# Kernel tuning notes

Measured on AMD Instinct MI355X. Metric: run time of the kernel, lower is better.

The kernel has to match this reference:

```python
import jax, jax.numpy as jnp
import numpy as np

C = 96        # channels
NH = 4        # num_heads
WIN = (2, 2, 2)
B, D, H, W = 2, 48, 48, 48
HID = 4 * C   # FFN hidden dim
EPS = 1e-5


def setup_inputs() -> dict:
    key = jax.random.key(0)
    ks = iter(jax.random.split(key, 64))
    def nrm(shape, scale=0.02):
        return jax.random.normal(next(ks), shape, jnp.float32) * scale
    inp = {
        "fg_feature": jax.random.normal(next(ks), (B, C, D, H, W), jnp.float32),
        "bg_feature": jax.random.normal(next(ks), (B, C, D, H, W), jnp.float32),
    }
    for p in ("fg", "bg"):
        inp[f"{p}_qn_w"] = jnp.ones((C,), jnp.float32)
        inp[f"{p}_qn_b"] = jnp.zeros((C,), jnp.float32)
        inp[f"{p}_kvn_w"] = jnp.ones((C,), jnp.float32)
        inp[f"{p}_kvn_b"] = jnp.zeros((C,), jnp.float32)
        inp[f"{p}_attn_in_w"] = nrm((3 * C, C))
        inp[f"{p}_attn_in_b"] = jnp.zeros((3 * C,), jnp.float32)
        inp[f"{p}_attn_out_w"] = nrm((C, C))
        inp[f"{p}_attn_out_b"] = jnp.zeros((C,), jnp.float32)
        inp[f"{p}_ffn_n_w"] = jnp.ones((C,), jnp.float32)
        inp[f"{p}_ffn_n_b"] = jnp.zeros((C,), jnp.float32)
        inp[f"{p}_ffn_w1"] = nrm((HID, C))
        inp[f"{p}_ffn_b1"] = jnp.zeros((HID,), jnp.float32)
        inp[f"{p}_ffn_w2"] = nrm((C, HID))
        inp[f"{p}_ffn_b2"] = jnp.zeros((C,), jnp.float32)
        inp[f"{p}_conv_w"] = nrm((C, C))  # 1x1x1 Conv3d kernel flattened to [Cout,Cin]
        inp[f"{p}_conv_b"] = jnp.zeros((C,), jnp.float32)
        inp[f"{p}_in_w"] = jnp.ones((C,), jnp.float32)
        inp[f"{p}_in_b"] = jnp.zeros((C,), jnp.float32)
    return inp


def _gelu(x):
    return jax.nn.gelu(x, approximate=False)  # torch nn.GELU default (erf)


def _ln(x, w, b):
    m = x.mean(-1, keepdims=True)
    v = ((x - m) ** 2).mean(-1, keepdims=True)
    return (x - m) * jax.lax.rsqrt(v + EPS) * w + b


def _window_partition(x):
    b, c, d, h, w = x.shape
    wd, wh, ww = WIN
    x = x.reshape(b, c, d // wd, wd, h // wh, wh, w // ww, ww)
    x = x.transpose(0, 2, 4, 6, 3, 5, 7, 1)
    return x.reshape(-1, wd * wh * ww, c)  # [num_windows, 8, C]


def _window_reverse(t, shape):
    b, c, d, h, w = shape
    wd, wh, ww = WIN
    x = t.reshape(b, d // wd, h // wh, w // ww, wd, wh, ww, c)
    x = x.transpose(0, 7, 1, 4, 2, 5, 3, 6)
    return x.reshape(b, c, d, h, w)


def _mha(q, k, v, Wi, bi, Wo, bo):
    # torch MultiheadAttention with packed in_proj, batch_first
    N, Lq, c = q.shape
    dh = c // NH
    qp = (q @ Wi[:c].T + bi[:c]).reshape(N, Lq, NH, dh)
    kp = (k @ Wi[c:2 * c].T + bi[c:2 * c]).reshape(N, -1, NH, dh)
    vp = (v @ Wi[2 * c:].T + bi[2 * c:]).reshape(N, -1, NH, dh)
    att = jnp.einsum('nqhd,nkhd->nhqk', qp, kp) * (1.0 / np.sqrt(dh))
    att = jax.nn.softmax(att, axis=-1)
    o = jnp.einsum('nhqk,nkhd->nqhd', att, vp).reshape(N, Lq, c)
    return o @ Wo.T + bo


def _ffn(x, w1, b1, w2, b2):
    return _gelu(x @ w1.T + b1) @ w2.T + b2


def _proj(x, cw, cb, iw, ib):
    # 1x1x1 Conv3d -> InstanceNorm3d(affine) -> GELU
    y = jnp.einsum('bcdhw,oc->bodhw', x, cw) + cb[None, :, None, None, None]
    m = y.mean((2, 3, 4), keepdims=True)
    v = ((y - m) ** 2).mean((2, 3, 4), keepdims=True)
    y = (y - m) * jax.lax.rsqrt(v + EPS)
    y = y * iw[None, :, None, None, None] + ib[None, :, None, None, None]
    return _gelu(y)


def _forward(fg_feature, bg_feature,
             fg_qn_w, fg_qn_b, fg_kvn_w, fg_kvn_b,
             fg_attn_in_w, fg_attn_in_b, fg_attn_out_w, fg_attn_out_b,
             fg_ffn_n_w, fg_ffn_n_b, fg_ffn_w1, fg_ffn_b1, fg_ffn_w2, fg_ffn_b2,
             fg_conv_w, fg_conv_b, fg_in_w, fg_in_b,
             bg_qn_w, bg_qn_b, bg_kvn_w, bg_kvn_b,
             bg_attn_in_w, bg_attn_in_b, bg_attn_out_w, bg_attn_out_b,
             bg_ffn_n_w, bg_ffn_n_b, bg_ffn_w1, bg_ffn_b1, bg_ffn_w2, bg_ffn_b2,
             bg_conv_w, bg_conv_b, bg_in_w, bg_in_b):
    meta = fg_feature.shape
    fg_t = _window_partition(fg_feature)
    bg_t = _window_partition(bg_feature)
    fg_q = _ln(fg_t, fg_qn_w, fg_qn_b)
    bg_q = _ln(bg_t, bg_qn_w, bg_qn_b)
    fg_c = _ln(fg_t, fg_kvn_w, fg_kvn_b)
    bg_c = _ln(bg_t, bg_kvn_w, bg_kvn_b)
    fg_t = fg_t + _mha(fg_q, bg_c, bg_c, fg_attn_in_w, fg_attn_in_b, fg_attn_out_w, fg_attn_out_b)
    bg_t = bg_t + _mha(bg_q, fg_c, fg_c, bg_attn_in_w, bg_attn_in_b, bg_attn_out_w, bg_attn_out_b)
    fg_t = fg_t + _ffn(_ln(fg_t, fg_ffn_n_w, fg_ffn_n_b), fg_ffn_w1, fg_ffn_b1, fg_ffn_w2, fg_ffn_b2)
    bg_t = bg_t + _ffn(_ln(bg_t, bg_ffn_n_w, bg_ffn_n_b), bg_ffn_w1, bg_ffn_b1, bg_ffn_w2, bg_ffn_b2)
    fg = _window_reverse(fg_t, meta)
    bg = _window_reverse(bg_t, meta)
    fg = _proj(fg, fg_conv_w, fg_conv_b, fg_in_w, fg_in_b)
    bg = _proj(bg, bg_conv_w, bg_conv_b, bg_in_w, bg_in_b)
    return fg, bg


def reference(fg_feature, bg_feature,
              fg_qn_w, fg_qn_b, fg_kvn_w, fg_kvn_b,
              fg_attn_in_w, fg_attn_in_b, fg_attn_out_w, fg_attn_out_b,
              fg_ffn_n_w, fg_ffn_n_b, fg_ffn_w1, fg_ffn_b1, fg_ffn_w2, fg_ffn_b2,
              fg_conv_w, fg_conv_b, fg_in_w, fg_in_b,
              bg_qn_w, bg_qn_b, bg_kvn_w, bg_kvn_b,
              bg_attn_in_w, bg_attn_in_b, bg_attn_out_w, bg_attn_out_b,
              bg_ffn_n_w, bg_ffn_n_b, bg_ffn_w1, bg_ffn_b1, bg_ffn_w2, bg_ffn_b2,
              bg_conv_w, bg_conv_b, bg_in_w, bg_in_b):
    return _forward(fg_feature, bg_feature,
                    fg_qn_w, fg_qn_b, fg_kvn_w, fg_kvn_b,
                    fg_attn_in_w, fg_attn_in_b, fg_attn_out_w, fg_attn_out_b,
                    fg_ffn_n_w, fg_ffn_n_b, fg_ffn_w1, fg_ffn_b1, fg_ffn_w2, fg_ffn_b2,
                    fg_conv_w, fg_conv_b, fg_in_w, fg_in_b,
                    bg_qn_w, bg_qn_b, bg_kvn_w, bg_kvn_b,
                    bg_attn_in_w, bg_attn_in_b, bg_attn_out_w, bg_attn_out_b,
                    bg_ffn_n_w, bg_ffn_n_b, bg_ffn_w1, bg_ffn_b1, bg_ffn_w2, bg_ffn_b2,
                    bg_conv_w, bg_conv_b, bg_in_w, bg_in_b)
```

## Files before the change

### kernel.cpp

```cpp
#include <hip/hip_runtime.h>
#include <hip/hip_bf16.h>


#define G_TOK 221184
#define TOK_PER_B 110592
#define STREAM_ELEMS 21233664

typedef __attribute__((ext_vector_type(8))) short short8;
typedef __attribute__((ext_vector_type(4))) float f32x4;
typedef unsigned short ushort_t;
typedef unsigned int uint_t;

#define MFMA16 __builtin_amdgcn_mfma_f32_16x16x32_bf16

__device__ __forceinline__ float gelu_erf(float x) {
    return 0.5f * x * (1.0f + erff(x * 0.70710678118654752f));
}
__device__ __forceinline__ float gelu_tanh(float x) {
    float u = x * (1.5957691216f + 0.0713548163f * x * x);
    return x / (1.0f + __expf(-u));
}
__device__ __forceinline__ ushort_t bfb(float f) {
    __hip_bfloat16 h = __float2bfloat16(f);
    return *reinterpret_cast<ushort_t*>(&h);
}
__device__ __forceinline__ void unpack8(uint4 v, float* o) {
    o[0] = __uint_as_float(v.x << 16); o[1] = __uint_as_float(v.x & 0xffff0000u);
    o[2] = __uint_as_float(v.y << 16); o[3] = __uint_as_float(v.y & 0xffff0000u);
    o[4] = __uint_as_float(v.z << 16); o[5] = __uint_as_float(v.z & 0xffff0000u);
    o[6] = __uint_as_float(v.w << 16); o[7] = __uint_as_float(v.w & 0xffff0000u);
}
__device__ __forceinline__ uint4 pack8(const float* f) {
    uint4 v;
    v.x = (uint_t)bfb(f[0]) | ((uint_t)bfb(f[1]) << 16);
    v.y = (uint_t)bfb(f[2]) | ((uint_t)bfb(f[3]) << 16);
    v.z = (uint_t)bfb(f[4]) | ((uint_t)bfb(f[5]) << 16);
    v.w = (uint_t)bfb(f[6]) | ((uint_t)bfb(f[7]) << 16);
    return v;
}
__device__ __forceinline__ uint2 pack4(const float* f) {
    uint2 v;
    v.x = (uint_t)bfb(f[0]) | ((uint_t)bfb(f[1]) << 16);
    v.y = (uint_t)bfb(f[2]) | ((uint_t)bfb(f[3]) << 16);
    return v;
}
__device__ __forceinline__ short8 pks8(const float* f) {
    short8 r;
    #pragma unroll
    for (int j = 0; j < 8; ++j) r[j] = (short)bfb(f[j]);
    return r;
}

__device__ __forceinline__ void stageAsync(ushort_t* dst, const ushort_t* src, int tid, int n16) {
    int wv = tid >> 6;
    #pragma unroll
    for (int i = 0; i < 2304; i += 256) {
        if (i >= n16) break;
        int idx = tid + i;
        if (idx < n16) {
            __builtin_amdgcn_global_load_lds(
                (const __attribute__((address_space(1))) uint_t*)((const uint4*)src + idx),
                (__attribute__((address_space(3))) uint_t*)(dst + (i + wv * 64) * 8),
                16, 0, 0);
        }
    }
}

__global__ __launch_bounds__(256) void k_fold(
    const float* __restrict__ Wi, const float* __restrict__ bi,
    const float* __restrict__ Wo, const float* __restrict__ bo,
    const float* __restrict__ W1, const float* __restrict__ b1,
    const float* __restrict__ W2, const float* __restrict__ b2,
    const float* __restrict__ Wc,
    const float* __restrict__ qnw, const float* __restrict__ qnb,
    const float* __restrict__ kvw, const float* __restrict__ kvb,
    const float* __restrict__ fnw, const float* __restrict__ fnb,
    ushort_t* __restrict__ w, float* __restrict__ bs)
{
    const float scale = 0.20412414523193150f;
    int tid0 = blockIdx.x * 256 + threadIdx.x;
    int nth = gridDim.x * 256;
    for (int o = tid0; o < 120672; o += nth) {
        if (o < 36864) {
            int blkid = o / 9216, oo = o % 9216;
            int e = oo & 7, ln = (oo >> 3) & 63, g = oo >> 9;
            int t = g / 3, u = g % 3, l15 = ln & 15, kb = ln >> 4;
            int c = t * 16 + l15, k = u * 32 + kb * 8 + e;
            float v;
            if (blkid == 0)      v = Wi[c * 96 + k] * qnw[k] * scale;
            else if (blkid == 1) v = Wi[(96 + c) * 96 + k] * kvw[k];
            else if (blkid == 2) v = Wi[(192 + c) * 96 + k] * kvw[k];
            else                 v = Wo[c * 96 + k];
            w[o] = bfb(v);
        } else if (o < 110592) {
            int oo = o - 36864; int half = oo / 36864; oo %= 36864;
            int e = oo & 7, ln = (oo >> 3) & 63, g = oo >> 9;
            int ch = g / 18, r = g % 18, tt = r / 3, u = r % 3;
            int l15 = ln & 15, kb = ln >> 4;
            float v;
            if (half == 0) {
                int c = ch * 96 + tt * 16 + l15, k = u * 32 + kb * 8 + e;
                v = W1[c * 96 + k] * fnw[k];
            } else {
                int c = tt * 16 + l15, k = ch * 96 + u * 32 + kb * 8 + e;
                v = W2[c * 384 + k];
            }
            w[o] = bfb(v);
        } else if (o < 119808) {
            int oo = o - 110592;
            int e = oo & 7, ln = (oo >> 3) & 63, g = oo >> 9;
            int t = g / 3, u = g % 3, l15 = ln & 15, kb = ln >> 4;
            w[o] = bfb(Wc[(t * 16 + l15) * 96 + u * 32 + kb * 8 + e]);
        } else {
            int x = o - 119808;
            if (x < 96) {
                float s = bi[x];
                #pragma unroll 4
                for (int k = 0; k < 96; ++k) s += qnb[k] * Wi[x * 96 + k];
                bs[x] = s * scale;
            } else if (x < 192) {
                int c = x - 96; float s = bi[96 + c];
                #pragma unroll 4
                for (int k = 0; k < 96; ++k) s += kvb[k] * Wi[(96 + c) * 96 + k];
                bs[x] = s;
            } else if (x < 288) {
                int c = x - 192; float s = bi[192 + c];
                #pragma unroll 4
                for (int k = 0; k < 96; ++k) s += kvb[k] * Wi[(192 + c) * 96 + k];
                bs[x] = s;
            } else if (x < 384) {
                bs[x] = bo[x - 288];
            } else if (x < 768) {
                int c = x - 384; float s = b1[c];
                #pragma unroll 4
                for (int k = 0; k < 96; ++k) s += fnb[k] * W1[c * 96 + k];
                bs[x] = s;
            } else {
                bs[x] = b2[x - 768];
            }
        }
    }
}

__global__ __launch_bounds__(256) void k_gather(
    const float* __restrict__ srcf, const float* __restrict__ srcb,
    ushort_t* __restrict__ Xf, ushort_t* __restrict__ Xb)
{
    __shared__ float tile[192 * 97];
    int blk = blockIdx.x;
    const float* src; ushort_t* X;
    if (blk < 1152) { src = srcf; X = Xf; }
    else            { src = srcb; X = Xb; blk -= 1152; }
    int b = blk / 576, rem = blk % 576, dw = rem / 24, hw = rem % 24;
    int tid = threadIdx.x;
    for (int i = tid; i < 384 * 48; i += 256) {
        int r = i / 48, w = i % 48;
        int c = r >> 2, d_off = (r >> 1) & 1, h_off = r & 1;
        float v = src[((((long)b * 96 + c) * 48 + dw * 2 + d_off) * 48 + hw * 2 + h_off) * 48 + w];
        int t = (w >> 1) * 8 + d_off * 4 + h_off * 2 + (w & 1);
        tile[t * 97 + c] = v;
    }
    __syncthreads();
    long base = ((((long)b * 24 + dw) * 24 + hw) * 24) * 8;
    for (int i = tid; i < 192 * 12; i += 256) {
        int t = i / 12, c8 = i % 12;
        *(uint4*)&X[(base + t) * 96 + c8 * 8] = pack8(&tile[t * 97 + c8 * 8]);
    }
}

__device__ __forceinline__ void gemmT_stage(
    const short8* xb2, const ushort_t* __restrict__ W,
    const float* __restrict__ bias, ushort_t* outs,
    int mbase, int l15, int kb)
{
    const int ln8 = (kb * 16 + l15) * 8;
    #pragma unroll
    for (int t = 0; t < 6; ++t) {
        float4 bv = *(const float4*)&bias[t * 16 + kb * 4];
        f32x4 A0 = {bv.x, bv.y, bv.z, bv.w};
        f32x4 A1 = {bv.x, bv.y, bv.z, bv.w};
        #pragma unroll
        for (int u = 0; u < 3; ++u) {
            short8 bw = *(const short8*)&W[(t * 3 + u) * 512 + ln8];
            A0 = MFMA16(bw, xb2[u],     A0, 0, 0, 0);
            A1 = MFMA16(bw, xb2[3 + u], A1, 0, 0, 0);
        }
        float f0[4], f1[4];
        #pragma unroll
        for (int i = 0; i < 4; ++i) { f0[i] = A0[i]; f1[i] = A1[i]; }
        *(uint2*)&outs[(mbase + l15) * 104 + t * 16 + kb * 4]      = pack4(f0);
        *(uint2*)&outs[(mbase + 16 + l15) * 104 + t * 16 + kb * 4] = pack4(f1);
    }
}

__global__ __launch_bounds__(256, 2) void k_attn(
    ushort_t* __restrict__ Xf, ushort_t* __restrict__ Xb,
    const ushort_t* __restrict__ wf, const ushort_t* __restrict__ wb,
    const float* __restrict__ bsf, const float* __restrict__ bsb)
{
    __shared__ ushort_t qs[128 * 104];
    __shared__ ushort_t kv[128 * 104];
    __shared__ ushort_t WB[9216];
    int tid = threadIdx.x, lane = tid & 63, wv = tid >> 6, mbase = wv * 32;
    int l15 = lane & 15, kb = lane >> 4;
    long g0 = (long)blockIdx.x * 128;

    short8 fr[2][6];
    #pragma unroll
    for (int s = 0; s < 2; ++s) {
        #pragma unroll
        for (int m = 0; m < 2; ++m) {
            const ushort_t* px = (s ? Xb : Xf) + (g0 + mbase + m * 16 + l15) * 96 + kb * 8;
            float f[24];
            unpack8(*(const uint4*)px, f);
            unpack8(*(const uint4*)(px + 32), f + 8);
            unpack8(*(const uint4*)(px + 64), f + 16);
            float s1 = 0.f, s2 = 0.f;
            #pragma unroll
            for (int j = 0; j < 24; ++j) { s1 += f[j]; s2 += f[j] * f[j]; }
            s1 += __shfl_xor(s1, 16); s1 += __shfl_xor(s1, 32);
            s2 += __shfl_xor(s2, 16); s2 += __shfl_xor(s2, 32);
            float mm = s1 * (1.f / 96.f);
            float rr = rsqrtf(s2 * (1.f / 96.f) - mm * mm + 1e-5f);
            #pragma unroll
            for (int j = 0; j < 24; ++j) f[j] = (f[j] - mm) * rr;
            fr[s][m * 3 + 0] = pks8(f);
            fr[s][m * 3 + 1] = pks8(f + 8);
            fr[s][m * 3 + 2] = pks8(f + 16);
        }
    }

    #pragma unroll
    for (int dir = 0; dir < 2; ++dir) {
        const ushort_t* W = dir ? wb : wf;
        const float* bs = dir ? bsb : bsf;
        ushort_t* X = dir ? Xb : Xf;

        stageAsync(WB, W + 9216, tid, 1152);
        gemmT_stage(fr[dir], W, bs, qs, mbase, l15, kb);
        __syncthreads();
        gemmT_stage(fr[dir ^ 1], WB, bs + 96, kv, mbase, l15, kb);

        float sc[2][8], inv[2];
        #pragma unroll
        for (int it = 0; it < 2; ++it) {
            int idx = lane + 64 * it;
            int win = (idx >> 5) & 3, hd = (idx >> 3) & 3, q8 = idx & 7;
            int tq = mbase + win * 8 + q8, ko = hd * 24;
            float qf[24];
            #pragma unroll
            for (int u = 0; u < 3; ++u)
                unpack8(*(const uint4*)&qs[tq * 104 + ko + u * 8], qf + u * 8);
            float mx = -1e30f;
            #pragma unroll
            for (int j = 0; j < 8; ++j) {
                float s = 0.f;
                #pragma unroll
                for (int u = 0; u < 3; ++u) {
                    float kf[8];
                    unpack8(*(const uint4*)&kv[(mbase + win * 8 + j) * 104 + ko + u * 8], kf);
                    #pragma unroll
                    for (int d = 0; d < 8; ++d) s += qf[u * 8 + d] * kf[d];
                }
                sc[it][j] = s; mx = fmaxf(mx, s);
            }
            float sum = 0.f;
            #pragma unroll
            for (int j = 0; j < 8; ++j) { sc[it][j] = __expf(sc[it][j] - mx); sum += sc[it][j]; }
            inv[it] = 1.f / sum;
        }
        __syncthreads();
        stageAsync(WB, W + 18432, tid, 1152);
        __syncthreads();
        gemmT_stage(fr[dir ^ 1], WB, bs + 192, kv, mbase, l15, kb);

        #pragma unroll
        for (int it = 0; it < 2; ++it) {
            int idx = lane + 64 * it;
            int win = (idx >> 5) & 3, hd = (idx >> 3) & 3, q8 = idx & 7;
            int tq = mbase + win * 8 + q8, ko = hd * 24;
            #pragma unroll
            for (int u = 0; u < 3; ++u) {
                float of8[8];
                #pragma unroll
                for (int d = 0; d < 8; ++d) of8[d] = 0.f;
                #pragma unroll
                for (int j = 0; j < 8; ++j) {
                    float vf[8];
                    unpack8(*(const uint4*)&kv[(mbase + win * 8 + j) * 104 + ko + u * 8], vf);
                    #pragma unroll
                    for (int d = 0; d < 8; ++d) of8[d] += sc[it][j] * vf[d];
                }
                #pragma unroll
                for (int d = 0; d < 8; ++d) of8[d] *= inv[it];
                *(uint4*)&qs[tq * 104 + ko + u * 8] = pack8(of8);
            }
        }
        __syncthreads();
        stageAsync(WB, W + 27648, tid, 1152);
        __syncthreads();
        {
            short8 o0[6];
            #pragma unroll
            for (int m = 0; m < 2; ++m)
                #pragma unroll
                for (int u = 0; u < 3; ++u)
                    o0[m * 3 + u] = *(const short8*)&qs[(mbase + m * 16 + l15) * 104 + u * 32 + kb * 8];
            gemmT_stage(o0, WB, bs + 288, qs, mbase, l15, kb);
        }
        #pragma unroll
        for (int u = 0; u < 6; ++u) {
            int idx = lane + 64 * u;
            int r2 = idx / 12, c8 = idx % 12;
            ushort_t* p = X + (g0 + mbase + r2) * 96 + c8 * 8;
            float xv[8], av[8], o[8];
            unpack8(*(const uint4*)p, xv);
            unpack8(*(const uint4*)&qs[(mbase + r2) * 104 + c8 * 8], av);
            #pragma unroll
            for (int j = 0; j < 8; ++j) o[j] = xv[j] + av[j];
            *(uint4*)p = pack8(o);
        }
        __syncthreads();
    }
}

__global__ __launch_bounds__(256, 2) void k_ffn(
    ushort_t* __restrict__ Xf, ushort_t* __restrict__ Xb,
    const ushort_t* __restrict__ wf, const ushort_t* __restrict__ wb,
    const float* __restrict__ bsf, const float* __restrict__ bsb)
{
    __shared__ ushort_t H[128 * 104];
    __shared__ ushort_t WB[18432];
    int blk = blockIdx.x, tid = threadIdx.x;
    ushort_t* X; const ushort_t* W; const float* bs;
    if (blk < 1728) { X = Xf; W = wf; bs = bsf; }
    else            { X = Xb; W = wb; bs = bsb; blk -= 1728; }
    long g0 = (long)blk * 128;
    int lane = tid & 63, wv = tid >> 6, mbase = wv * 32;
    int l15 = lane & 15, kb = lane >> 4;
    const int ln8 = lane * 8;

    stageAsync(WB, W + 36864, tid, 1152);
    stageAsync(WB + 9216, W + 73728, tid, 1152);

    short8 xb2[6];
    #pragma unroll
    for (int m = 0; m < 2; ++m) {
        const ushort_t* px = X + (g0 + mbase + m * 16 + l15) * 96 + kb * 8;
        float f[24];
        unpack8(*(const uint4*)px, f);
        unpack8(*(const uint4*)(px + 32), f + 8);
        unpack8(*(const uint4*)(px + 64), f + 16);
        float s1 = 0.f, s2 = 0.f;
        #pragma unroll
        for (int j = 0; j < 24; ++j) { s1 += f[j]; s2 += f[j] * f[j]; }
        s1 += __shfl_xor(s1, 16); s1 += __shfl_xor(s1, 32);
        s2 += __shfl_xor(s2, 16); s2 += __shfl_xor(s2, 32);
        float mm = s1 * (1.f / 96.f);
        float rr = rsqrtf(s2 * (1.f / 96.f) - mm * mm + 1e-5f);
        #pragma unroll
        for (int j = 0; j < 24; ++j) f[j] = (f[j] - mm) * rr;
        xb2[m * 3 + 0] = pks8(f); xb2[m * 3 + 1] = pks8(f + 8); xb2[m * 3 + 2] = pks8(f + 16);
    }

    const ushort_t* W1 = W + 36864;
    const ushort_t* W2 = W + 73728;
    const ushort_t* Wc = W + 110592;
    const float* b1 = bs + 384;
    const float* b2 = bs + 768;

    f32x4 acc2[2][6];
    #pragma unroll
    for (int t = 0; t < 6; ++t) {
        float4 bv = *(const float4*)&b2[t * 16 + kb * 4];
        acc2[0][t] = {bv.x, bv.y, bv.z, bv.w};
        acc2[1][t] = {bv.x, bv.y, bv.z, bv.w};
    }
    for (int ch = 0; ch < 4; ++ch) {
        __syncthreads();
        #pragma unroll
        for (int t = 0; t < 6; ++t) {
            float4 bv = *(const float4*)&b1[ch * 96 + t * 16 + kb * 4];
            f32x4 A0 = {bv.x, bv.y, bv.z, bv.w};
            f32x4 A1 = {bv.x, bv.y, bv.z, bv.w};
            #pragma unroll
            for (int u = 0; u < 3; ++u) {
                short8 bw = *(const short8*)&WB[(t * 3 + u) * 512 + ln8];
                A0 = MFMA16(bw, xb2[u],     A0, 0, 0, 0);
                A1 = MFMA16(bw, xb2[3 + u], A1, 0, 0, 0);
            }
            float q0[4], q1[4];
            #pragma unroll
            for (int i = 0; i < 4; ++i) { q0[i] = gelu_tanh(A0[i]); q1[i] = gelu_tanh(A1[i]); }
            *(uint2*)&H[(mbase + l15) * 104 + t * 16 + kb * 4]      = pack4(q0);
            *(uint2*)&H[(mbase + 16 + l15) * 104 + t * 16 + kb * 4] = pack4(q1);
        }
        short8 h0[3], h1[3];
        #pragma unroll
        for (int u = 0; u < 3; ++u) {
            h0[u] = *(const short8*)&H[(mbase + l15) * 104 + u * 32 + kb * 8];
            h1[u] = *(const short8*)&H[(mbase + 16 + l15) * 104 + u * 32 + kb * 8];
        }
        #pragma unroll
        for (int t = 0; t < 6; ++t) {
            #pragma unroll
            for (int u = 0; u < 3; ++u) {
                short8 bw = *(const short8*)&WB[9216 + (t * 3 + u) * 512 + ln8];
                acc2[0][t] = MFMA16(bw, h0[u], acc2[0][t], 0, 0, 0);
                acc2[1][t] = MFMA16(bw, h1[u], acc2[1][t], 0, 0, 0);
            }
        }
        __syncthreads();
        if (ch < 3) {
            stageAsync(WB, W1 + (ch + 1) * 9216, tid, 1152);
            stageAsync(WB + 9216, W2 + (ch + 1) * 9216, tid, 1152);
        } else {
            stageAsync(WB, Wc, tid, 1152);
        }
    }
    #pragma unroll
    for (int t = 0; t < 6; ++t) {
        float f0[4], f1[4];
        #pragma unroll
        for (int i = 0; i < 4; ++i) { f0[i] = acc2[0][t][i]; f1[i] = acc2[1][t][i]; }
        *(uint2*)&H[(mbase + l15) * 104 + t * 16 + kb * 4]      = pack4(f0);
        *(uint2*)&H[(mbase + 16 + l15) * 104 + t * 16 + kb * 4] = pack4(f1);
    }
    #pragma unroll
    for (int u = 0; u < 6; ++u) {
        int idx = lane + 64 * u;
        int r2 = idx / 12, c8 = idx % 12;
        float xv[8], fv[8], y[8];
        unpack8(*(const uint4*)(X + (g0 + mbase + r2) * 96 + c8 * 8), xv);
        unpack8(*(const uint4*)&H[(mbase + r2) * 104 + c8 * 8], fv);
        #pragma unroll
        for (int j = 0; j < 8; ++j) y[j] = xv[j] + fv[j];
        *(uint4*)&H[(mbase + r2) * 104 + c8 * 8] = pack8(y);
    }
    __syncthreads();
    short8 y0[3], y1[3];
    #pragma unroll
    for (int u = 0; u < 3; ++u) {
        y0[u] = *(const short8*)&H[(mbase + l15) * 104 + u * 32 + kb * 8];
        y1[u] = *(const short8*)&H[(mbase + 16 + l15) * 104 + u * 32 + kb * 8];
    }
    #pragma unroll
    for (int t = 0; t < 6; ++t) {
        f32x4 A0 = {0.f, 0.f, 0.f, 0.f}, A1 = {0.f, 0.f, 0.f, 0.f};
        #pragma unroll
        for (int u = 0; u < 3; ++u) {
            short8 bw = *(const short8*)&WB[(t * 3 + u) * 512 + ln8];
            A0 = MFMA16(bw, y0[u], A0, 0, 0, 0);
            A1 = MFMA16(bw, y1[u], A1, 0, 0, 0);
        }
        float o0[4], o1[4];
        #pragma unroll
        for (int i = 0; i < 4; ++i) { o0[i] = A0[i]; o1[i] = A1[i]; }
        *(uint2*)&H[(mbase + l15) * 104 + t * 16 + kb * 4]      = pack4(o0);
        *(uint2*)&H[(mbase + 16 + l15) * 104 + t * 16 + kb * 4] = pack4(o1);
    }
    #pragma unroll
    for (int u = 0; u < 6; ++u) {
        int idx = lane + 64 * u;
        int r2 = idx / 12, c8 = idx % 12;
        *(uint4*)(X + (g0 + mbase + r2) * 96 + c8 * 8) =
            *(const uint4*)&H[(mbase + r2) * 104 + c8 * 8];
    }
}

__global__ __launch_bounds__(384) void k_instats(
    const ushort_t* __restrict__ Xf, const ushort_t* __restrict__ Xb,
    float* __restrict__ partial)
{
    __shared__ float red[2][32][96];
    int blk = blockIdx.x;
    const ushort_t* X = (blk < 108) ? Xf : Xb;
    int rem = blk % 108;
    int b = rem / 54, chunk = rem % 54;
    int tid = threadIdx.x;
    int c8 = tid % 12, slot = tid / 12;
    long base = (long)b * TOK_PER_B + chunk * 2048;
    float s8[8], ss8[8];
    #pragma unroll
    for (int j = 0; j < 8; ++j) { s8[j] = 0.f; ss8[j] = 0.f; }
    for (int i = 0; i < 64; ++i) {
        long row = base + i * 32 + slot;
        float f[8];
        unpack8(*(const uint4*)&X[row * 96 + c8 * 8], f);
        #pragma unroll
        for (int j = 0; j < 8; ++j) { s8[j] += f[j]; ss8[j] += f[j] * f[j]; }
    }
    #pragma unroll
    for (int j = 0; j < 8; ++j) {
        red[0][slot][c8 * 8 + j] = s8[j];
        red[1][slot][c8 * 8 + j] = ss8[j];
    }
    __syncthreads();
    if (tid < 96) {
        float S = 0.f, SS = 0.f;
        for (int sl = 0; sl < 32; ++sl) { S += red[0][sl][tid]; SS += red[1][sl][tid]; }
        partial[((long)blockIdx.x * 96 + tid) * 2]     = S;
        partial[((long)blockIdx.x * 96 + tid) * 2 + 1] = SS;
    }
}

__global__ __launch_bounds__(384) void k_infin(
    const float* __restrict__ partial, float* __restrict__ inMR)
{
    int tid = threadIdx.x;
    int s = tid / 192, rem = tid % 192, b = rem / 96, c = rem % 96;
    float S = 0.f, SS = 0.f;
    for (int ch = 0; ch < 54; ++ch) {
        int blk = s * 108 + b * 54 + ch;
        S  += partial[(blk * 96 + c) * 2];
        SS += partial[(blk * 96 + c) * 2 + 1];
    }
    float m = S * (1.f / 110592.f);
    float var = SS * (1.f / 110592.f) - m * m;
    inMR[tid * 2] = m;
    inMR[tid * 2 + 1] = rsqrtf(var + 1e-5f);
}

__global__ __launch_bounds__(256) void k_scatter(
    const ushort_t* __restrict__ Xf, const ushort_t* __restrict__ Xb,
    const float* __restrict__ inMR,
    const float* __restrict__ iwf, const float* __restrict__ ibf,
    const float* __restrict__ iwb, const float* __restrict__ ibb,
    float* __restrict__ out)
{
    __shared__ float tile[192 * 97];
    int blk = blockIdx.x, s = 0;
    const ushort_t* X = Xf; const float* iw = iwf; const float* ib = ibf;
    if (blk >= 1152) { s = 1; X = Xb; iw = iwb; ib = ibb; blk -= 1152; }
    int b = blk / 576, rem = blk % 576, dw = rem / 24, hw = rem % 24;
    int tid = threadIdx.x;
    long base = ((((long)b * 24 + dw) * 24 + hw) * 24) * 8;
    for (int i = tid; i < 192 * 12; i += 256) {
        int t = i / 12, c8 = i % 12;
        float f[8]; unpack8(*(const uint4*)&X[(base + t) * 96 + c8 * 8], f);
        #pragma unroll
        for (int j = 0; j < 8; ++j) tile[t * 97 + c8 * 8 + j] = f[j];
    }
    __syncthreads();
    float* o = out + (long)s * STREAM_ELEMS;
    for (int i = tid; i < 384 * 48; i += 256) {
        int r = i / 48, w = i % 48;
        int c = r >> 2, d_off = (r >> 1) & 1, h_off = r & 1;
        int t = (w >> 1) * 8 + d_off * 4 + h_off * 2 + (w & 1);
        float v = tile[t * 97 + c];
        float m  = inMR[((s * 2 + b) * 96 + c) * 2];
        float rr = inMR[((s * 2 + b) * 96 + c) * 2 + 1];
        v = (v - m) * rr * iw[c] + ib[c];
        o[((((long)b * 96 + c) * 48 + dw * 2 + d_off) * 48 + hw * 2 + h_off) * 48 + w] = gelu_erf(v);
    }
}

extern "C" void kernel_launch(void* const* d_in, const int* in_sizes, int n_in,
                              void* d_out, int out_size, void* d_ws, size_t ws_size,
                              hipStream_t stream)
{
    #define IN(i) ((const float*)d_in[i])
    ushort_t* Xf = (ushort_t*)d_ws;
    ushort_t* Xb = Xf + (long)STREAM_ELEMS;
    ushort_t* wW  = Xb + (long)STREAM_ELEMS;
    ushort_t* wWb = wW + 119808;
    float* bsf = (float*)(wWb + 119808);
    float* bsb = bsf + 864;
    float* partial = bsb + 864;
    float* inMR = partial + 41472;

    k_fold<<<128, 256, 0, stream>>>(IN(6), IN(7), IN(8), IN(9), IN(12), IN(13), IN(14), IN(15), IN(16),
                                    IN(2), IN(3), IN(22), IN(23), IN(10), IN(11), wW, bsf);
    k_fold<<<128, 256, 0, stream>>>(IN(24), IN(25), IN(26), IN(27), IN(30), IN(31), IN(32), IN(33), IN(34),
                                    IN(20), IN(21), IN(4), IN(5), IN(28), IN(29), wWb, bsb);

    k_gather<<<2304, 256, 0, stream>>>(IN(0), IN(1), Xf, Xb);

    k_attn<<<1728, 256, 0, stream>>>(Xf, Xb, wW, wWb, bsf, bsb);

    k_ffn<<<3456, 256, 0, stream>>>(Xf, Xb, wW, wWb, bsf, bsb);

    k_instats<<<216, 384, 0, stream>>>(Xf, Xb, partial);
    k_infin<<<1, 384, 0, stream>>>(partial, inMR);

    k_scatter<<<2304, 256, 0, stream>>>(Xf, Xb, inMR,
                                        IN(18), IN(19), IN(36), IN(37),
                                        (float*)d_out);
    #undef IN
}
```

Before: 532.7 us.

## Read MFMA weight fragments directly from global memory instead of LDS staging

Removes the async global-to-LDS staging of weight tiles in the attention and FFN kernels, so MFMA B-operands are loaded straight from global memory (served by L2/L1 cache) and most block-wide barriers go away. Dropping the LDS weight buffers reduces shared-memory use, and the FFN kernel's occupancy hint is raised from 2 to 3 blocks per CU. The trade-off is more global/cache load traffic and latency on the MFMA inner loops in exchange for fewer syncs and higher occupancy. The barriers that remained protect only per-wave rows of LDS, so removing them relies on each wave touching its own region.

```diff
diff --git a/kernel.cpp b/kernel.cpp
--- a/kernel.cpp
+++ b/kernel.cpp
@@ -49,21 +49,6 @@
     #pragma unroll
     for (int j = 0; j < 8; ++j) r[j] = (short)bfb(f[j]);
     return r;
-}
-
-__device__ __forceinline__ void stageAsync(ushort_t* dst, const ushort_t* src, int tid, int n16) {
-    int wv = tid >> 6;
-    #pragma unroll
-    for (int i = 0; i < 2304; i += 256) {
-        if (i >= n16) break;
-        int idx = tid + i;
-        if (idx < n16) {
-            __builtin_amdgcn_global_load_lds(
-                (const __attribute__((address_space(1))) uint_t*)((const uint4*)src + idx),
-                (__attribute__((address_space(3))) uint_t*)(dst + (i + wv * 64) * 8),
-                16, 0, 0);
-        }
-    }
 }
 
 __global__ __launch_bounds__(256) void k_fold(
@@ -200,7 +185,6 @@
 {
     __shared__ ushort_t qs[128 * 104];
     __shared__ ushort_t kv[128 * 104];
-    __shared__ ushort_t WB[9216];
     int tid = threadIdx.x, lane = tid & 63, wv = tid >> 6, mbase = wv * 32;
     int l15 = lane & 15, kb = lane >> 4;
     long g0 = (long)blockIdx.x * 128;
@@ -236,10 +220,8 @@
         const float* bs = dir ? bsb : bsf;
         ushort_t* X = dir ? Xb : Xf;
 
-        stageAsync(WB, W + 9216, tid, 1152);
-        gemmT_stage(fr[dir], W, bs, qs, mbase, l15, kb);
-        __syncthreads();
-        gemmT_stage(fr[dir ^ 1], WB, bs + 96, kv, mbase, l15, kb);
+        gemmT_stage(fr[dir],     W,        bs,      qs, mbase, l15, kb);
+        gemmT_stage(fr[dir ^ 1], W + 9216, bs + 96, kv, mbase, l15, kb);
 
         float sc[2][8], inv[2];
         #pragma unroll
@@ -269,10 +251,8 @@
             for (int j = 0; j < 8; ++j) { sc[it][j] = __expf(sc[it][j] - mx); sum += sc[it][j]; }
             inv[it] = 1.f / sum;
         }
-        __syncthreads();
-        stageAsync(WB, W + 18432, tid, 1152);
-        __syncthreads();
-        gemmT_stage(fr[dir ^ 1], WB, bs + 192, kv, mbase, l15, kb);
+
+        gemmT_stage(fr[dir ^ 1], W + 18432, bs + 192, kv, mbase, l15, kb);
 
         #pragma unroll
         for (int it = 0; it < 2; ++it) {
@@ -296,9 +276,7 @@
                 *(uint4*)&qs[tq * 104 + ko + u * 8] = pack8(of8);
             }
         }
-        __syncthreads();
-        stageAsync(WB, W + 27648, tid, 1152);
-        __syncthreads();
+
         {
             short8 o0[6];
             #pragma unroll
@@ -306,7 +284,7 @@
                 #pragma unroll
                 for (int u = 0; u < 3; ++u)
                     o0[m * 3 + u] = *(const short8*)&qs[(mbase + m * 16 + l15) * 104 + u * 32 + kb * 8];
-            gemmT_stage(o0, WB, bs + 288, qs, mbase, l15, kb);
+            gemmT_stage(o0, W + 27648, bs + 288, qs, mbase, l15, kb);
         }
         #pragma unroll
         for (int u = 0; u < 6; ++u) {
@@ -320,17 +298,15 @@
             for (int j = 0; j < 8; ++j) o[j] = xv[j] + av[j];
             *(uint4*)p = pack8(o);
         }
-        __syncthreads();
-    }
-}
-
-__global__ __launch_bounds__(256, 2) void k_ffn(
+    }
+}
+
+__global__ __launch_bounds__(256, 3) void k_ffn(
     ushort_t* __restrict__ Xf, ushort_t* __restrict__ Xb,
     const ushort_t* __restrict__ wf, const ushort_t* __restrict__ wb,
     const float* __restrict__ bsf, const float* __restrict__ bsb)
 {
     __shared__ ushort_t H[128 * 104];
-    __shared__ ushort_t WB[18432];
     int blk = blockIdx.x, tid = threadIdx.x;
     ushort_t* X; const ushort_t* W; const float* bs;
     if (blk < 1728) { X = Xf; W = wf; bs = bsf; }
@@ -340,9 +316,6 @@
     int l15 = lane & 15, kb = lane >> 4;
     const int ln8 = lane * 8;
 
-    stageAsync(WB, W + 36864, tid, 1152);
-    stageAsync(WB + 9216, W + 73728, tid, 1152);
-
     short8 xb2[6];
     #pragma unroll
     for (int m = 0; m < 2; ++m) {
@@ -376,8 +349,8 @@
         acc2[0][t] = {bv.x, bv.y, bv.z, bv.w};
         acc2[1][t] = {bv.x, bv.y, bv.z, bv.w};
     }
+    #pragma unroll
     for (int ch = 0; ch < 4; ++ch) {
-        __syncthreads();
         #pragma unroll
         for (int t = 0; t < 6; ++t) {
             float4 bv = *(const float4*)&b1[ch * 96 + t * 16 + kb * 4];
@@ -385,7 +358,7 @@
             f32x4 A1 = {bv.x, bv.y, bv.z, bv.w};
             #pragma unroll
             for (int u = 0; u < 3; ++u) {
-                short8 bw = *(const short8*)&WB[(t * 3 + u) * 512 + ln8];
+                short8 bw = *(const short8*)&W1[(ch * 18 + t * 3 + u) * 512 + ln8];
                 A0 = MFMA16(bw, xb2[u],     A0, 0, 0, 0);
                 A1 = MFMA16(bw, xb2[3 + u], A1, 0, 0, 0);
             }
@@ -405,17 +378,10 @@
         for (int t = 0; t < 6; ++t) {
             #pragma unroll
             for (int u = 0; u < 3; ++u) {
-                short8 bw = *(const short8*)&WB[9216 + (t * 3 + u) * 512 + ln8];
+                short8 bw = *(const short8*)&W2[(ch * 18 + t * 3 + u) * 512 + ln8];
                 acc2[0][t] = MFMA16(bw, h0[u], acc2[0][t], 0, 0, 0);
                 acc2[1][t] = MFMA16(bw, h1[u], acc2[1][t], 0, 0, 0);
             }
-        }
-        __syncthreads();
-        if (ch < 3) {
-            stageAsync(WB, W1 + (ch + 1) * 9216, tid, 1152);
-            stageAsync(WB + 9216, W2 + (ch + 1) * 9216, tid, 1152);
-        } else {
-            stageAsync(WB, Wc, tid, 1152);
         }
     }
     #pragma unroll
@@ -437,7 +403,6 @@
         for (int j = 0; j < 8; ++j) y[j] = xv[j] + fv[j];
         *(uint4*)&H[(mbase + r2) * 104 + c8 * 8] = pack8(y);
     }
-    __syncthreads();
     short8 y0[3], y1[3];
     #pragma unroll
     for (int u = 0; u < 3; ++u) {
@@ -449,7 +414,7 @@
         f32x4 A0 = {0.f, 0.f, 0.f, 0.f}, A1 = {0.f, 0.f, 0.f, 0.f};
         #pragma unroll
         for (int u = 0; u < 3; ++u) {
-            short8 bw = *(const short8*)&WB[(t * 3 + u) * 512 + ln8];
+            short8 bw = *(const short8*)&Wc[(t * 3 + u) * 512 + ln8];
             A0 = MFMA16(bw, y0[u], A0, 0, 0, 0);
             A1 = MFMA16(bw, y1[u], A1, 0, 0, 0);
         }
```

New measurement: 659.8 us. +23.8%, slower.
